# Kernel optimization log

Hardware: AMD Instinct MI355X
Metric: run time of the kernel (lower is better)

The kernel has to match this reference:

```python
import jax, jax.numpy as jnp
import numpy as np

N_NODES = 100000
N_EDGES = 1600000
IN_F = 32
HID = 128


def setup_inputs() -> dict:
    key = jax.random.key(0)
    ks = jax.random.split(key, 8)
    x = jax.random.normal(ks[0], (N_NODES, IN_F), dtype=jnp.float32)
    edge_index = jax.random.randint(ks[1], (2, N_EDGES), 0, N_NODES, dtype=jnp.int64)
    # Glorot-ish scaled weights
    W1 = jax.random.normal(ks[2], (IN_F, HID), dtype=jnp.float32) / np.sqrt(IN_F)
    b1 = jnp.zeros((HID,), dtype=jnp.float32)
    W2 = jax.random.normal(ks[3], (HID, HID), dtype=jnp.float32) / np.sqrt(HID)
    b2 = jnp.zeros((HID,), dtype=jnp.float32)
    W3 = jax.random.normal(ks[4], (HID, IN_F), dtype=jnp.float32) / np.sqrt(HID)
    b3 = jnp.zeros((IN_F,), dtype=jnp.float32)
    return {"x": x, "edge_index": edge_index, "W1": W1, "b1": b1,
            "W2": W2, "b2": b2, "W3": W3, "b3": b3}


def _gcn_norm(edge_index, n_nodes):
    # Add self-loops (PyG GCNConv default) and compute symmetric normalization
    loops = jnp.arange(n_nodes, dtype=edge_index.dtype)
    src = jnp.concatenate([edge_index[0], loops])
    dst = jnp.concatenate([edge_index[1], loops])
    ones = jnp.ones(src.shape[0], dtype=jnp.float32)
    deg = jax.ops.segment_sum(ones, dst, num_segments=n_nodes)
    deg_inv_sqrt = jnp.where(deg > 0, jax.lax.rsqrt(deg), 0.0)
    norm = deg_inv_sqrt[src] * deg_inv_sqrt[dst]  # [E + N]
    return src, dst, norm


def _gcn_conv(x, src, dst, norm, W, b, n_nodes):
    h = x @ W                                # [N, out] transform first (smaller msgs when out<in)
    msg = h[src] * norm[:, None]             # gather + edge-wise scale  [E+N, out]
    out = jax.ops.segment_sum(msg, dst, num_segments=n_nodes)  # scatter-add
    return out + b


def reference(x, edge_index, W1, b1, W2, b2, W3, b3):
    n = x.shape[0]
    src, dst, norm = _gcn_norm(edge_index, n)
    h = jax.nn.relu(_gcn_conv(x, src, dst, norm, W1, b1, n))
    h = jax.nn.relu(_gcn_conv(h, src, dst, norm, W2, b2, n))
    h = jax.nn.relu(_gcn_conv(h, src, dst, norm, W3, b3, n))
    return h
```

## Files before the change

kernel.cpp:

```cpp
#include <hip/hip_runtime.h>
#include <hip/hip_fp16.h>

#define N_NODES 100000
#define N_EDGES 1600000
#define IN_F 32
#define HID 128
#define NBLK_SCAN 391
#define BSHIFT 9
#define BSIZE 512
#define NBUCK 196
#define EPB 2048
#define NBB 782

typedef _Float16 half8 __attribute__((ext_vector_type(8)));
typedef float floatx4 __attribute__((ext_vector_type(4)));

static __device__ __forceinline__ void pack2(_Float16* dst, float a, float b) {
    union { _Float16 h[2]; unsigned u; } p;
    p.h[0] = (_Float16)a; p.h[1] = (_Float16)b;
    *(unsigned*)dst = p.u;
}


__global__ void k_zero_ideg(int* __restrict__ ideg) {
    int i = blockIdx.x * 256 + threadIdx.x;
    if (i < N_NODES) ideg[i] = 0;
}

__global__ void k_count(const int* __restrict__ dst, int* __restrict__ ideg) {
    int e = blockIdx.x * 256 + threadIdx.x;
    if (e < N_EDGES) atomicAdd(&ideg[dst[e]], 1);
}

__global__ __launch_bounds__(256) void k_scan1(const int* __restrict__ ideg,
                                               int* __restrict__ cursor,
                                               int* __restrict__ partials) {
    __shared__ int s[256];
    int gid = blockIdx.x * 256 + threadIdx.x;
    int v = (gid < N_NODES) ? ideg[gid] : 0;
    s[threadIdx.x] = v;
    __syncthreads();
    for (int off = 1; off < 256; off <<= 1) {
        int t = (threadIdx.x >= off) ? s[threadIdx.x - off] : 0;
        __syncthreads();
        s[threadIdx.x] += t;
        __syncthreads();
    }
    if (gid < N_NODES) cursor[gid] = s[threadIdx.x] - v;
    if (threadIdx.x == 255) partials[blockIdx.x] = s[255];
}

__global__ __launch_bounds__(512) void k_scan2(int* __restrict__ partials) {
    __shared__ int s[512];
    int v = (threadIdx.x < NBLK_SCAN) ? partials[threadIdx.x] : 0;
    s[threadIdx.x] = v;
    __syncthreads();
    for (int off = 1; off < 512; off <<= 1) {
        int t = (threadIdx.x >= off) ? s[threadIdx.x - off] : 0;
        __syncthreads();
        s[threadIdx.x] += t;
        __syncthreads();
    }
    if (threadIdx.x < NBLK_SCAN) partials[threadIdx.x] = s[threadIdx.x] - v;
}

__global__ void k_scan3(int* __restrict__ cursor, const int* __restrict__ partials) {
    int gid = blockIdx.x * 256 + threadIdx.x;
    if (gid < N_NODES) cursor[gid] += partials[blockIdx.x];
}

__global__ void k_binit(const int* __restrict__ cursor, int* __restrict__ bcur) {
    int t = threadIdx.x;
    if (t < NBUCK) bcur[t] = cursor[t << BSHIFT];
}

__global__ __launch_bounds__(256) void k_bucket(const int* __restrict__ src,
                                                const int* __restrict__ dst,
                                                int* __restrict__ bcur,
                                                unsigned* __restrict__ rec) {
    __shared__ int hist[256];
    __shared__ int lbase[256];
    const int e0 = blockIdx.x * EPB;
    hist[threadIdx.x] = 0;
    __syncthreads();

    unsigned rk[8]; int bk[8];
#pragma unroll
    for (int k = 0; k < 8; ++k) {
        int e = e0 + k * 256 + threadIdx.x;
        if (e < N_EDGES) {
            int d = dst[e];
            int b = d >> BSHIFT;
            bk[k] = b;
            rk[k] = ((unsigned)src[e] << BSHIFT) | (unsigned)(d & (BSIZE - 1));
            atomicAdd(&hist[b], 1);
        } else bk[k] = -1;
    }
    __syncthreads();
    int c = hist[threadIdx.x];
    lbase[threadIdx.x] = (c > 0) ? atomicAdd(&bcur[threadIdx.x], c) : 0;
    __syncthreads();
    hist[threadIdx.x] = 0;
    __syncthreads();
#pragma unroll
    for (int k = 0; k < 8; ++k) {
        if (bk[k] >= 0) {
            int off = atomicAdd(&hist[bk[k]], 1);
            rec[lbase[bk[k]] + off] = rk[k];
        }
    }
}

__global__ __launch_bounds__(256) void k_fill2(const int* __restrict__ cursor,
                                               const unsigned* __restrict__ rec,
                                               int* __restrict__ col) {
    __shared__ int lcur[BSIZE];
    const int b = blockIdx.x;
    const int n0 = b << BSHIFT;
    for (int t = threadIdx.x; t < BSIZE; t += 256) {
        int n = n0 + t;
        lcur[t] = (n < N_NODES) ? cursor[n] : 0;
    }
    const int rbeg = cursor[n0];
    const int rend = (b == NBUCK - 1) ? N_EDGES : cursor[n0 + BSIZE];
    __syncthreads();
    for (int i = rbeg + threadIdx.x; i < rend; i += 256) {
        unsigned r = rec[i];
        int slot = atomicAdd(&lcur[r & (BSIZE - 1)], 1);
        col[slot] = (int)(r >> BSHIFT);
    }
}


__global__ void k_prescale(const float2* __restrict__ x, const int* __restrict__ ideg,
                           __half2* __restrict__ T) {
    int tid = blockIdx.x * 256 + threadIdx.x;
    if (tid >= N_NODES * 16) return;
    int i = tid >> 4;
    float dis = rsqrtf(1.0f + (float)ideg[i]);
    float2 v = x[tid];
    T[tid] = __floats2half2_rn(v.x * dis, v.y * dis);
}


__global__ __launch_bounds__(256) void k_gather32h_pre(
    const int* __restrict__ cursor, const int* __restrict__ ideg,
    const int* __restrict__ col, const __half2* __restrict__ T,
    float2* __restrict__ OUT) {
    int node = blockIdx.x * 16 + (threadIdx.x >> 4);
    int j = threadIdx.x & 15;
    if (node >= N_NODES) return;
    int e   = cursor[node];
    int d   = ideg[node];
    int end = e + d;
    float2 acc = __half22float2(T[(size_t)node * 16 + j]);
    for (; e + 3 < end; e += 4) {
        int s0 = col[e], s1 = col[e + 1], s2 = col[e + 2], s3 = col[e + 3];
        float2 f0 = __half22float2(T[(size_t)s0 * 16 + j]);
        float2 f1 = __half22float2(T[(size_t)s1 * 16 + j]);
        float2 f2 = __half22float2(T[(size_t)s2 * 16 + j]);
        float2 f3 = __half22float2(T[(size_t)s3 * 16 + j]);
        acc.x += (f0.x + f1.x) + (f2.x + f3.x);
        acc.y += (f0.y + f1.y) + (f2.y + f3.y);
    }
    for (; e < end; ++e) {
        float2 f = __half22float2(T[(size_t)col[e] * 16 + j]);
        acc.x += f.x; acc.y += f.y;
    }
    float dis = rsqrtf(1.0f + (float)d);
    OUT[(size_t)node * 16 + j] = make_float2(acc.x * dis, acc.y * dis);
}

__global__ __launch_bounds__(256) void k_gather32h_fin(
    const int* __restrict__ cursor, const int* __restrict__ ideg,
    const int* __restrict__ col, const __half2* __restrict__ T,
    const float* __restrict__ b, float2* __restrict__ OUT) {
    int node = blockIdx.x * 16 + (threadIdx.x >> 4);
    int j = threadIdx.x & 15;
    if (node >= N_NODES) return;
    int e   = cursor[node];
    int d   = ideg[node];
    int end = e + d;
    float2 acc = __half22float2(T[(size_t)node * 16 + j]);
    for (; e + 3 < end; e += 4) {
        int s0 = col[e], s1 = col[e + 1], s2 = col[e + 2], s3 = col[e + 3];
        float2 f0 = __half22float2(T[(size_t)s0 * 16 + j]);
        float2 f1 = __half22float2(T[(size_t)s1 * 16 + j]);
        float2 f2 = __half22float2(T[(size_t)s2 * 16 + j]);
        float2 f3 = __half22float2(T[(size_t)s3 * 16 + j]);
        acc.x += (f0.x + f1.x) + (f2.x + f3.x);
        acc.y += (f0.y + f1.y) + (f2.y + f3.y);
    }
    for (; e < end; ++e) {
        float2 f = __half22float2(T[(size_t)col[e] * 16 + j]);
        acc.x += f.x; acc.y += f.y;
    }
    float dis = rsqrtf(1.0f + (float)d);
    float vx = acc.x * dis + b[2 * j];
    float vy = acc.y * dis + b[2 * j + 1];
    OUT[(size_t)node * 16 + j] =
        make_float2(vx > 0.f ? vx : 0.f, vy > 0.f ? vy : 0.f);
}

__global__ __launch_bounds__(256) void k_gather128h(
    const int* __restrict__ cursor, const int* __restrict__ ideg,
    const int* __restrict__ col, const __half2* __restrict__ T,
    const float* __restrict__ b, __half2* __restrict__ OUT) {
    int node = blockIdx.x * 4 + (threadIdx.x >> 6);
    int j = threadIdx.x & 63;
    if (node >= N_NODES) return;
    int e   = cursor[node];
    int d   = ideg[node];
    int end = e + d;
    float2 acc = __half22float2(T[(size_t)node * 64 + j]);
    for (; e + 3 < end; e += 4) {
        int s0 = col[e], s1 = col[e + 1], s2 = col[e + 2], s3 = col[e + 3];
        float2 f0 = __half22float2(T[(size_t)s0 * 64 + j]);
        float2 f1 = __half22float2(T[(size_t)s1 * 64 + j]);
        float2 f2 = __half22float2(T[(size_t)s2 * 64 + j]);
        float2 f3 = __half22float2(T[(size_t)s3 * 64 + j]);
        acc.x += (f0.x + f1.x) + (f2.x + f3.x);
        acc.y += (f0.y + f1.y) + (f2.y + f3.y);
    }
    for (; e < end; ++e) {
        float2 f = __half22float2(T[(size_t)col[e] * 64 + j]);
        acc.x += f.x; acc.y += f.y;
    }
    float dis = rsqrtf(1.0f + (float)d);
    float vx = acc.x * dis + b[2 * j];
    float vy = acc.y * dis + b[2 * j + 1];
    OUT[(size_t)node * 64 + j] =
        __floats2half2_rn(vx > 0.f ? vx : 0.f, vy > 0.f ? vy : 0.f);
}


__global__ __launch_bounds__(256) void k_xform1_mfma(
    const float* __restrict__ z, const float* __restrict__ W,
    const float* __restrict__ bias, _Float16* __restrict__ Hh) {
    __shared__ _Float16 Wt[128 * 40];
    for (int idx = threadIdx.x; idx < 2048; idx += 256) {
        int n = idx & 127, k = (idx >> 7) * 2;
        pack2(&Wt[n * 40 + k], W[k * HID + n], W[(k + 1) * HID + n]);
    }
    __syncthreads();

    const int lane = threadIdx.x & 63;
    const int wave = threadIdx.x >> 6;
    const int m16 = lane & 15, quad = lane >> 4;
    const int row0 = blockIdx.x * 64 + wave * 16;
    if (row0 >= N_NODES) return;

    int arow = row0 + m16; if (arow >= N_NODES) arow = N_NODES - 1;
    const float* zp = z + (size_t)arow * IN_F + quad * 8;
    float4 z0 = *(const float4*)zp;
    float4 z1 = *(const float4*)(zp + 4);
    half8 a = {(_Float16)z0.x, (_Float16)z0.y, (_Float16)z0.z, (_Float16)z0.w,
               (_Float16)z1.x, (_Float16)z1.y, (_Float16)z1.z, (_Float16)z1.w};

    floatx4 acc[8];
#pragma unroll
    for (int t = 0; t < 8; ++t) acc[t] = (floatx4){0.f, 0.f, 0.f, 0.f};
#pragma unroll
    for (int t = 0; t < 8; ++t) {
        half8 b = *(const half8*)&Wt[(t * 16 + m16) * 40 + quad * 8];
        acc[t] = __builtin_amdgcn_mfma_f32_16x16x32_f16(a, b, acc[t], 0, 0, 0);
    }
#pragma unroll
    for (int t = 0; t < 8; ++t) {
        int c = t * 16 + m16;
        float bj = bias[c];
#pragma unroll
        for (int r = 0; r < 4; ++r) {
            int row = row0 + quad * 4 + r;
            if (row < N_NODES) {
                float v = acc[t][r] + bj;
                Hh[(size_t)row * HID + c] = (_Float16)(v > 0.f ? v : 0.f);
            }
        }
    }
}

__global__ __launch_bounds__(256) void k_xform2_mfma(
    const _Float16* __restrict__ H, const float* __restrict__ W,
    const int* __restrict__ ideg, _Float16* __restrict__ T) {
    __shared__ _Float16 Wt[128 * 136];
    for (int idx = threadIdx.x; idx < 8192; idx += 256) {
        int n = idx & 127, k = (idx >> 7) * 2;
        pack2(&Wt[n * 136 + k], W[k * HID + n], W[(k + 1) * HID + n]);
    }
    __syncthreads();

    const int lane = threadIdx.x & 63;
    const int wave = threadIdx.x >> 6;
    const int m16 = lane & 15, quad = lane >> 4;
    const int row0 = blockIdx.x * 64 + wave * 16;
    if (row0 >= N_NODES) return;

    int arow = row0 + m16; if (arow >= N_NODES) arow = N_NODES - 1;
    const _Float16* hp = H + (size_t)arow * HID + quad * 8;
    half8 a[4];
#pragma unroll
    for (int kk = 0; kk < 4; ++kk) a[kk] = *(const half8*)(hp + kk * 32);

    floatx4 acc[8];
#pragma unroll
    for (int t = 0; t < 8; ++t) acc[t] = (floatx4){0.f, 0.f, 0.f, 0.f};
#pragma unroll
    for (int t = 0; t < 8; ++t) {
        const _Float16* wp = &Wt[(t * 16 + m16) * 136 + quad * 8];
#pragma unroll
        for (int kk = 0; kk < 4; ++kk) {
            half8 b = *(const half8*)(wp + kk * 32);
            acc[t] = __builtin_amdgcn_mfma_f32_16x16x32_f16(a[kk], b, acc[t], 0, 0, 0);
        }
    }
    float dis[4];
#pragma unroll
    for (int r = 0; r < 4; ++r) {
        int row = row0 + quad * 4 + r;
        dis[r] = (row < N_NODES) ? rsqrtf(1.0f + (float)ideg[row]) : 0.f;
    }
#pragma unroll
    for (int t = 0; t < 8; ++t) {
        int c = t * 16 + m16;
#pragma unroll
        for (int r = 0; r < 4; ++r) {
            int row = row0 + quad * 4 + r;
            if (row < N_NODES)
                T[(size_t)row * HID + c] = (_Float16)(acc[t][r] * dis[r]);
        }
    }
}

__global__ __launch_bounds__(256) void k_xform3_mfma(
    const _Float16* __restrict__ H, const float* __restrict__ W,
    const int* __restrict__ ideg, _Float16* __restrict__ T) {
    __shared__ _Float16 Wt[32 * 136];
    for (int idx = threadIdx.x; idx < 2048; idx += 256) {
        int n = idx & 31, k = (idx >> 5) * 2;
        pack2(&Wt[n * 136 + k], W[k * IN_F + n], W[(k + 1) * IN_F + n]);
    }
    __syncthreads();

    const int lane = threadIdx.x & 63;
    const int wave = threadIdx.x >> 6;
    const int m16 = lane & 15, quad = lane >> 4;
    const int row0 = blockIdx.x * 64 + wave * 16;
    if (row0 >= N_NODES) return;

    int arow = row0 + m16; if (arow >= N_NODES) arow = N_NODES - 1;
    const _Float16* hp = H + (size_t)arow * HID + quad * 8;
    half8 a[4];
#pragma unroll
    for (int kk = 0; kk < 4; ++kk) a[kk] = *(const half8*)(hp + kk * 32);

    floatx4 acc[2];
#pragma unroll
    for (int t = 0; t < 2; ++t) acc[t] = (floatx4){0.f, 0.f, 0.f, 0.f};
#pragma unroll
    for (int t = 0; t < 2; ++t) {
        const _Float16* wp = &Wt[(t * 16 + m16) * 136 + quad * 8];
#pragma unroll
        for (int kk = 0; kk < 4; ++kk) {
            half8 b = *(const half8*)(wp + kk * 32);
            acc[t] = __builtin_amdgcn_mfma_f32_16x16x32_f16(a[kk], b, acc[t], 0, 0, 0);
        }
    }
    float dis[4];
#pragma unroll
    for (int r = 0; r < 4; ++r) {
        int row = row0 + quad * 4 + r;
        dis[r] = (row < N_NODES) ? rsqrtf(1.0f + (float)ideg[row]) : 0.f;
    }
#pragma unroll
    for (int t = 0; t < 2; ++t) {
        int c = t * 16 + m16;
#pragma unroll
        for (int r = 0; r < 4; ++r) {
            int row = row0 + quad * 4 + r;
            if (row < N_NODES)
                T[(size_t)row * IN_F + c] = (_Float16)(acc[t][r] * dis[r]);
        }
    }
}


extern "C" void kernel_launch(void* const* d_in, const int* in_sizes, int n_in,
                              void* d_out, int out_size, void* d_ws, size_t ws_size,
                              hipStream_t stream) {
    const float* x  = (const float*)d_in[0];
    const int*   ei = (const int*)d_in[1];
    const float* W1 = (const float*)d_in[2];
    const float* b1 = (const float*)d_in[3];
    const float* W2 = (const float*)d_in[4];
    const float* b2 = (const float*)d_in[5];
    const float* W3 = (const float*)d_in[6];
    const float* b3 = (const float*)d_in[7];
    float* out = (float*)d_out;

    const int* src = ei;
    const int* dst = ei + N_EDGES;

    int*      ideg     = (int*)d_ws;
    int*      cursor   = ideg + 102400;
    int*      partials = cursor + 102400;
    int*      bcur     = partials + 512;
    int*      col      = bcur + 256;
    unsigned* rec      = (unsigned*)(col + N_EDGES);
    __half2*  t1h      = (__half2*)(rec + N_EDGES);
    float*    z        = (float*)(t1h + (size_t)N_NODES * 16);
    _Float16* H1h      = (_Float16*)(z + (size_t)N_NODES * IN_F);
    _Float16* T2h      = H1h + (size_t)N_NODES * HID;
    _Float16* H2h      = T2h + (size_t)N_NODES * HID;

    const int xgrid = (N_NODES + 63) / 64;

    k_zero_ideg<<<NBLK_SCAN, 256, 0, stream>>>(ideg);
    k_count<<<(N_EDGES + 255) / 256, 256, 0, stream>>>(dst, ideg);
    k_scan1<<<NBLK_SCAN, 256, 0, stream>>>(ideg, cursor, partials);
    k_scan2<<<1, 512, 0, stream>>>(partials);
    k_scan3<<<NBLK_SCAN, 256, 0, stream>>>(cursor, partials);
    k_binit<<<1, 256, 0, stream>>>(cursor, bcur);
    k_bucket<<<NBB, 256, 0, stream>>>(src, dst, bcur, rec);
    k_fill2<<<NBUCK, 256, 0, stream>>>(cursor, rec, col);

    k_prescale<<<(N_NODES * 16 + 255) / 256, 256, 0, stream>>>(
        (const float2*)x, ideg, t1h);
    k_gather32h_pre<<<(N_NODES + 15) / 16, 256, 0, stream>>>(
        cursor, ideg, col, t1h, (float2*)z);
    k_xform1_mfma<<<xgrid, 256, 0, stream>>>(z, W1, b1, H1h);

    k_xform2_mfma<<<xgrid, 256, 0, stream>>>(H1h, W2, ideg, T2h);
    k_gather128h<<<(N_NODES + 3) / 4, 256, 0, stream>>>(
        cursor, ideg, col, (const __half2*)T2h, b2, (__half2*)H2h);

    k_xform3_mfma<<<xgrid, 256, 0, stream>>>(H2h, W3, ideg, T2h);
    k_gather32h_fin<<<(N_NODES + 15) / 16, 256, 0, stream>>>(
        cursor, ideg, col, (const __half2*)T2h, b3, (float2*)out);
}
```

Before: 390.6 us.

## Split gather edges across wave lanes with 16-byte loads and shuffle reduction

All three SpMM gather kernels are rewritten so each wave processes one node at a time in a grid-stride loop. Lanes split the edges into parallel slots, each loading 16-byte half8 row chunks, and partial sums are combined with xor shuffles. Previously each lane walked all edges serially with 4-byte loads. The first-layer aggregate is now stored as fp16 instead of fp32, which halves its traffic and lets xform1 load it directly. Separately, the bucketing kernel processes 8192 edges per block with short bucket ids to reduce global atomics on bucket cursors; this raises register pressure, and the shuffle reduction adds work for low-degree nodes.

```diff
diff --git a/kernel.cpp b/kernel.cpp
--- a/kernel.cpp
+++ b/kernel.cpp
@@ -9,8 +9,8 @@
 #define BSHIFT 9
 #define BSIZE 512
 #define NBUCK 196
-#define EPB 2048
-#define NBB 782
+#define EPB 8192
+#define NBB 196
 
 typedef _Float16 half8 __attribute__((ext_vector_type(8)));
 typedef float floatx4 __attribute__((ext_vector_type(4)));
@@ -84,14 +84,14 @@
     hist[threadIdx.x] = 0;
     __syncthreads();
 
-    unsigned rk[8]; int bk[8];
-#pragma unroll
-    for (int k = 0; k < 8; ++k) {
+    unsigned rk[32]; short bk[32];
+#pragma unroll
+    for (int k = 0; k < 32; ++k) {
         int e = e0 + k * 256 + threadIdx.x;
         if (e < N_EDGES) {
             int d = dst[e];
             int b = d >> BSHIFT;
-            bk[k] = b;
+            bk[k] = (short)b;
             rk[k] = ((unsigned)src[e] << BSHIFT) | (unsigned)(d & (BSIZE - 1));
             atomicAdd(&hist[b], 1);
         } else bk[k] = -1;
@@ -103,7 +103,7 @@
     hist[threadIdx.x] = 0;
     __syncthreads();
 #pragma unroll
-    for (int k = 0; k < 8; ++k) {
+    for (int k = 0; k < 32; ++k) {
         if (bk[k] >= 0) {
             int off = atomicAdd(&hist[bk[k]], 1);
             rec[lbase[bk[k]] + off] = rk[k];
@@ -143,99 +143,171 @@
 }
 
 
-__global__ __launch_bounds__(256) void k_gather32h_pre(
+__global__ __launch_bounds__(256) void k_gather32_pre(
     const int* __restrict__ cursor, const int* __restrict__ ideg,
-    const int* __restrict__ col, const __half2* __restrict__ T,
-    float2* __restrict__ OUT) {
-    int node = blockIdx.x * 16 + (threadIdx.x >> 4);
-    int j = threadIdx.x & 15;
-    if (node >= N_NODES) return;
-    int e   = cursor[node];
-    int d   = ideg[node];
-    int end = e + d;
-    float2 acc = __half22float2(T[(size_t)node * 16 + j]);
-    for (; e + 3 < end; e += 4) {
-        int s0 = col[e], s1 = col[e + 1], s2 = col[e + 2], s3 = col[e + 3];
-        float2 f0 = __half22float2(T[(size_t)s0 * 16 + j]);
-        float2 f1 = __half22float2(T[(size_t)s1 * 16 + j]);
-        float2 f2 = __half22float2(T[(size_t)s2 * 16 + j]);
-        float2 f3 = __half22float2(T[(size_t)s3 * 16 + j]);
-        acc.x += (f0.x + f1.x) + (f2.x + f3.x);
-        acc.y += (f0.y + f1.y) + (f2.y + f3.y);
-    }
-    for (; e < end; ++e) {
-        float2 f = __half22float2(T[(size_t)col[e] * 16 + j]);
-        acc.x += f.x; acc.y += f.y;
-    }
-    float dis = rsqrtf(1.0f + (float)d);
-    OUT[(size_t)node * 16 + j] = make_float2(acc.x * dis, acc.y * dis);
-}
-
-__global__ __launch_bounds__(256) void k_gather32h_fin(
+    const int* __restrict__ col, const _Float16* __restrict__ T,
+    _Float16* __restrict__ OUT) {
+    const int lane = threadIdx.x & 63;
+    const int slot = lane >> 2;
+    const int fl   = lane & 3;
+    const int wid  = blockIdx.x * 4 + (threadIdx.x >> 6);
+    const int wstride = gridDim.x * 4;
+
+    for (int node = wid; node < N_NODES; node += wstride) {
+        int begin = cursor[node];
+        int d     = ideg[node];
+        int end   = begin + d;
+        float acc[8];
+        if (slot == 0) {
+            half8 v = *(const half8*)(T + (size_t)node * IN_F + fl * 8);
+#pragma unroll
+            for (int i = 0; i < 8; ++i) acc[i] = (float)v[i];
+        } else {
+#pragma unroll
+            for (int i = 0; i < 8; ++i) acc[i] = 0.f;
+        }
+        for (int e = begin; e < end; e += 16) {
+            int ee = e + slot;
+            if (ee < end) {
+                int s = col[ee];
+                half8 v = *(const half8*)(T + (size_t)s * IN_F + fl * 8);
+#pragma unroll
+                for (int i = 0; i < 8; ++i) acc[i] += (float)v[i];
+            }
+        }
+#pragma unroll
+        for (int m = 4; m < 64; m <<= 1)
+#pragma unroll
+            for (int i = 0; i < 8; ++i) acc[i] += __shfl_xor(acc[i], m, 64);
+        if (slot == 0) {
+            float dis = rsqrtf(1.0f + (float)d);
+            half8 o;
+#pragma unroll
+            for (int i = 0; i < 8; ++i) o[i] = (_Float16)(acc[i] * dis);
+            *(half8*)(OUT + (size_t)node * IN_F + fl * 8) = o;
+        }
+    }
+}
+
+__global__ __launch_bounds__(256) void k_gather32_fin(
     const int* __restrict__ cursor, const int* __restrict__ ideg,
-    const int* __restrict__ col, const __half2* __restrict__ T,
-    const float* __restrict__ b, float2* __restrict__ OUT) {
-    int node = blockIdx.x * 16 + (threadIdx.x >> 4);
-    int j = threadIdx.x & 15;
-    if (node >= N_NODES) return;
-    int e   = cursor[node];
-    int d   = ideg[node];
-    int end = e + d;
-    float2 acc = __half22float2(T[(size_t)node * 16 + j]);
-    for (; e + 3 < end; e += 4) {
-        int s0 = col[e], s1 = col[e + 1], s2 = col[e + 2], s3 = col[e + 3];
-        float2 f0 = __half22float2(T[(size_t)s0 * 16 + j]);
-        float2 f1 = __half22float2(T[(size_t)s1 * 16 + j]);
-        float2 f2 = __half22float2(T[(size_t)s2 * 16 + j]);
-        float2 f3 = __half22float2(T[(size_t)s3 * 16 + j]);
-        acc.x += (f0.x + f1.x) + (f2.x + f3.x);
-        acc.y += (f0.y + f1.y) + (f2.y + f3.y);
-    }
-    for (; e < end; ++e) {
-        float2 f = __half22float2(T[(size_t)col[e] * 16 + j]);
-        acc.x += f.x; acc.y += f.y;
-    }
-    float dis = rsqrtf(1.0f + (float)d);
-    float vx = acc.x * dis + b[2 * j];
-    float vy = acc.y * dis + b[2 * j + 1];
-    OUT[(size_t)node * 16 + j] =
-        make_float2(vx > 0.f ? vx : 0.f, vy > 0.f ? vy : 0.f);
-}
-
-__global__ __launch_bounds__(256) void k_gather128h(
+    const int* __restrict__ col, const _Float16* __restrict__ T,
+    const float* __restrict__ b, float* __restrict__ OUT) {
+    const int lane = threadIdx.x & 63;
+    const int slot = lane >> 2;
+    const int fl   = lane & 3;
+    const int wid  = blockIdx.x * 4 + (threadIdx.x >> 6);
+    const int wstride = gridDim.x * 4;
+
+    float4 bb0 = *(const float4*)(b + fl * 8);
+    float4 bb1 = *(const float4*)(b + fl * 8 + 4);
+    float bias[8] = {bb0.x, bb0.y, bb0.z, bb0.w, bb1.x, bb1.y, bb1.z, bb1.w};
+
+    for (int node = wid; node < N_NODES; node += wstride) {
+        int begin = cursor[node];
+        int d     = ideg[node];
+        int end   = begin + d;
+        float acc[8];
+        if (slot == 0) {
+            half8 v = *(const half8*)(T + (size_t)node * IN_F + fl * 8);
+#pragma unroll
+            for (int i = 0; i < 8; ++i) acc[i] = (float)v[i];
+        } else {
+#pragma unroll
+            for (int i = 0; i < 8; ++i) acc[i] = 0.f;
+        }
+        for (int e = begin; e < end; e += 16) {
+            int ee = e + slot;
+            if (ee < end) {
+                int s = col[ee];
+                half8 v = *(const half8*)(T + (size_t)s * IN_F + fl * 8);
+#pragma unroll
+                for (int i = 0; i < 8; ++i) acc[i] += (float)v[i];
+            }
+        }
+#pragma unroll
+        for (int m = 4; m < 64; m <<= 1)
+#pragma unroll
+            for (int i = 0; i < 8; ++i) acc[i] += __shfl_xor(acc[i], m, 64);
+        if (slot == 0) {
+            float dis = rsqrtf(1.0f + (float)d);
+            float o[8];
+#pragma unroll
+            for (int i = 0; i < 8; ++i) {
+                float v = acc[i] * dis + bias[i];
+                o[i] = v > 0.f ? v : 0.f;
+            }
+            float* op = OUT + (size_t)node * IN_F + fl * 8;
+            *(float4*)op       = make_float4(o[0], o[1], o[2], o[3]);
+            *(float4*)(op + 4) = make_float4(o[4], o[5], o[6], o[7]);
+        }
+    }
+}
+
+__global__ __launch_bounds__(256) void k_gather128(
     const int* __restrict__ cursor, const int* __restrict__ ideg,
-    const int* __restrict__ col, const __half2* __restrict__ T,
-    const float* __restrict__ b, __half2* __restrict__ OUT) {
-    int node = blockIdx.x * 4 + (threadIdx.x >> 6);
-    int j = threadIdx.x & 63;
-    if (node >= N_NODES) return;
-    int e   = cursor[node];
-    int d   = ideg[node];
-    int end = e + d;
-    float2 acc = __half22float2(T[(size_t)node * 64 + j]);
-    for (; e + 3 < end; e += 4) {
-        int s0 = col[e], s1 = col[e + 1], s2 = col[e + 2], s3 = col[e + 3];
-        float2 f0 = __half22float2(T[(size_t)s0 * 64 + j]);
-        float2 f1 = __half22float2(T[(size_t)s1 * 64 + j]);
-        float2 f2 = __half22float2(T[(size_t)s2 * 64 + j]);
-        float2 f3 = __half22float2(T[(size_t)s3 * 64 + j]);
-        acc.x += (f0.x + f1.x) + (f2.x + f3.x);
-        acc.y += (f0.y + f1.y) + (f2.y + f3.y);
-    }
-    for (; e < end; ++e) {
-        float2 f = __half22float2(T[(size_t)col[e] * 64 + j]);
-        acc.x += f.x; acc.y += f.y;
-    }
-    float dis = rsqrtf(1.0f + (float)d);
-    float vx = acc.x * dis + b[2 * j];
-    float vy = acc.y * dis + b[2 * j + 1];
-    OUT[(size_t)node * 64 + j] =
-        __floats2half2_rn(vx > 0.f ? vx : 0.f, vy > 0.f ? vy : 0.f);
+    const int* __restrict__ col, const _Float16* __restrict__ T,
+    const float* __restrict__ b, _Float16* __restrict__ OUT) {
+    const int lane = threadIdx.x & 63;
+    const int slot = lane >> 4;
+    const int fl   = lane & 15;
+    const int wid  = blockIdx.x * 4 + (threadIdx.x >> 6);
+    const int wstride = gridDim.x * 4;
+
+    float4 bb0 = *(const float4*)(b + fl * 8);
+    float4 bb1 = *(const float4*)(b + fl * 8 + 4);
+    float bias[8] = {bb0.x, bb0.y, bb0.z, bb0.w, bb1.x, bb1.y, bb1.z, bb1.w};
+
+    for (int node = wid; node < N_NODES; node += wstride) {
+        int begin = cursor[node];
+        int d     = ideg[node];
+        int end   = begin + d;
+        float acc[8];
+        if (slot == 0) {
+            half8 v = *(const half8*)(T + (size_t)node * HID + fl * 8);
+#pragma unroll
+            for (int i = 0; i < 8; ++i) acc[i] = (float)v[i];
+        } else {
+#pragma unroll
+            for (int i = 0; i < 8; ++i) acc[i] = 0.f;
+        }
+        for (int e = begin; e < end; e += 8) {
+            int ee0 = e + slot;
+            int ee1 = e + 4 + slot;
+            if (ee1 < end) {
+                int s0 = col[ee0];
+                int s1 = col[ee1];
+                half8 v0 = *(const half8*)(T + (size_t)s0 * HID + fl * 8);
+                half8 v1 = *(const half8*)(T + (size_t)s1 * HID + fl * 8);
+#pragma unroll
+                for (int i = 0; i < 8; ++i) acc[i] += (float)v0[i] + (float)v1[i];
+            } else if (ee0 < end) {
+                int s0 = col[ee0];
+                half8 v0 = *(const half8*)(T + (size_t)s0 * HID + fl * 8);
+#pragma unroll
+                for (int i = 0; i < 8; ++i) acc[i] += (float)v0[i];
+            }
+        }
+#pragma unroll
+        for (int m = 16; m < 64; m <<= 1)
+#pragma unroll
+            for (int i = 0; i < 8; ++i) acc[i] += __shfl_xor(acc[i], m, 64);
+        if (slot == 0) {
+            float dis = rsqrtf(1.0f + (float)d);
+            half8 o;
+#pragma unroll
+            for (int i = 0; i < 8; ++i) {
+                float v = acc[i] * dis + bias[i];
+                o[i] = (_Float16)(v > 0.f ? v : 0.f);
+            }
+            *(half8*)(OUT + (size_t)node * HID + fl * 8) = o;
+        }
+    }
 }
 
 
 __global__ __launch_bounds__(256) void k_xform1_mfma(
-    const float* __restrict__ z, const float* __restrict__ W,
+    const _Float16* __restrict__ z, const float* __restrict__ W,
     const float* __restrict__ bias, _Float16* __restrict__ Hh) {
     __shared__ _Float16 Wt[128 * 40];
     for (int idx = threadIdx.x; idx < 2048; idx += 256) {
@@ -251,11 +323,7 @@
     if (row0 >= N_NODES) return;
 
     int arow = row0 + m16; if (arow >= N_NODES) arow = N_NODES - 1;
-    const float* zp = z + (size_t)arow * IN_F + quad * 8;
-    float4 z0 = *(const float4*)zp;
-    float4 z1 = *(const float4*)(zp + 4);
-    half8 a = {(_Float16)z0.x, (_Float16)z0.y, (_Float16)z0.z, (_Float16)z0.w,
-               (_Float16)z1.x, (_Float16)z1.y, (_Float16)z1.z, (_Float16)z1.w};
+    half8 a = *(const half8*)(z + (size_t)arow * IN_F + quad * 8);
 
     floatx4 acc[8];
 #pragma unroll
@@ -407,9 +475,9 @@
     int*      bcur     = partials + 512;
     int*      col      = bcur + 256;
     unsigned* rec      = (unsigned*)(col + N_EDGES);
-    __half2*  t1h      = (__half2*)(rec + N_EDGES);
-    float*    z        = (float*)(t1h + (size_t)N_NODES * 16);
-    _Float16* H1h      = (_Float16*)(z + (size_t)N_NODES * IN_F);
+    _Float16* t1h      = (_Float16*)(rec + N_EDGES);
+    _Float16* z        = t1h + (size_t)N_NODES * IN_F;
+    _Float16* H1h      = z + (size_t)N_NODES * IN_F;
     _Float16* T2h      = H1h + (size_t)N_NODES * HID;
     _Float16* H2h      = T2h + (size_t)N_NODES * HID;
 
@@ -425,16 +493,13 @@
     k_fill2<<<NBUCK, 256, 0, stream>>>(cursor, rec, col);
 
     k_prescale<<<(N_NODES * 16 + 255) / 256, 256, 0, stream>>>(
-        (const float2*)x, ideg, t1h);
-    k_gather32h_pre<<<(N_NODES + 15) / 16, 256, 0, stream>>>(
-        cursor, ideg, col, t1h, (float2*)z);
+        (const float2*)x, ideg, (__half2*)t1h);
+    k_gather32_pre<<<2048, 256, 0, stream>>>(cursor, ideg, col, t1h, z);
     k_xform1_mfma<<<xgrid, 256, 0, stream>>>(z, W1, b1, H1h);
 
     k_xform2_mfma<<<xgrid, 256, 0, stream>>>(H1h, W2, ideg, T2h);
-    k_gather128h<<<(N_NODES + 3) / 4, 256, 0, stream>>>(
-        cursor, ideg, col, (const __half2*)T2h, b2, (__half2*)H2h);
+    k_gather128<<<2048, 256, 0, stream>>>(cursor, ideg, col, T2h, b2, H2h);
 
     k_xform3_mfma<<<xgrid, 256, 0, stream>>>(H2h, W3, ideg, T2h);
-    k_gather32h_fin<<<(N_NODES + 15) / 16, 256, 0, stream>>>(
-        cursor, ideg, col, (const __half2*)T2h, b3, (float2*)out);
-}
+    k_gather32_fin<<<2048, 256, 0, stream>>>(cursor, ideg, col, T2h, b3, out);
+}
```

Result: no change. 386.1 us (-1.2%).
